# Kernel optimization log

Measured on AMD Instinct MI355X. Metric: run time of the kernel, lower is better.

The kernel has to match this reference:

```python
import jax, jax.numpy as jnp
import numpy as np

C, M, D, B, BG_KNN = 8, 2048, 2048, 256, 50
TEMP, MOMENTUM = 0.05, 0.2


def setup_inputs() -> dict:
    key = jax.random.key(0)
    k1, k2, k3, k4 = jax.random.split(key, 4)
    inputs = jax.random.normal(k1, (B, D), jnp.float32)
    inputs = inputs / jnp.linalg.norm(inputs, axis=1, keepdims=True)  # ReID feats are L2-normed
    em = jax.random.normal(k2, (C * M, D), jnp.float32)
    em = em / jnp.linalg.norm(em, axis=1, keepdims=True)  # memory rows are kept unit-norm
    targets = jax.random.randint(k3, (B,), 0, M)          # global pseudo labels in [0, M)
    cams = jax.random.randint(k4, (B,), 0, C).astype(jnp.int32)
    return {"inputs": inputs, "em": em, "targets": targets, "cams": cams, "epoch": 6}


def _loss(inputs, em_sg, targets, cams, epoch):
    em3 = em_sg.reshape(C, M, D)
    loss = jnp.zeros((), jnp.float32)
    # per-camera intra-camera cross entropy (ExemplarMemory fwd: inputs @ em.T / temp)
    for cc in range(C):
        mask = (cams == cc)
        cnt = jnp.maximum(mask.sum(), 1).astype(jnp.float32)
        logits = (inputs @ em3[cc].T) / TEMP                       # [B, M]
        logp = jax.nn.log_softmax(logits, axis=1)
        ce = -jnp.take_along_axis(logp, targets[:, None], axis=1)[:, 0]
        loss = loss + jnp.where(mask.any(), jnp.where(mask, ce, 0.0).sum() / cnt, 0.0)
    if epoch >= 5:
        sims = inputs @ em_sg.T                                    # [B, C*M]
        # positives: one proxy per camera at row target + M*c
        pos_ind = targets[:, None] + M * jnp.arange(C)[None, :]    # [B, C]
        pos_logits = jnp.take_along_axis(sims, pos_ind, axis=1) / TEMP
        masked = jax.lax.stop_gradient(sims).at[jnp.arange(B)[:, None], pos_ind].set(-1000.0)
        _, neg_ind = jax.lax.top_k(masked, BG_KNN)                 # bg_knn hard negatives
        neg_logits = jnp.take_along_axis(sims, neg_ind, axis=1) / TEMP
        cat = jnp.concatenate([pos_logits, neg_logits], axis=1)   # [B, C+BG_KNN]
        logp = jax.nn.log_softmax(cat, axis=1)
        al = -logp[:, :C].mean(axis=1)                             # weights 1/#pos on positives
        for cc in range(C):
            mask = (cams == cc)
            cnt = jnp.maximum(mask.sum(), 1).astype(jnp.float32)
            loss = loss + jnp.where(mask.any(), 0.5 * jnp.where(mask, al, 0.0).sum() / cnt, 0.0)
    return loss


def reference(inputs, em, targets, cams, epoch):
    em_sg = jax.lax.stop_gradient(em)  # memory is a buffer: no grad flows to it in torch
    loss = _loss(inputs, em_sg, targets, cams, int(epoch))
    # sequential per-sample EMA scatter update + renorm (torch does this in backward)
    rows = cams.astype(jnp.int32) * M + targets.astype(jnp.int32)
    x_sg = jax.lax.stop_gradient(inputs)

    def step(em_cur, xr):
        x, r = xr
        row = MOMENTUM * em_cur[r] + (1.0 - MOMENTUM) * x
        row = row / jnp.linalg.norm(row)
        return em_cur.at[r].set(row), None

    em_new, _ = jax.lax.scan(step, em_sg, (x_sg, rows))
    return loss, em_new
```

## Files before the change

### kernel.cpp

```cpp
#include <hip/hip_runtime.h>

#define Bn   256
#define Dk   2048
#define Cc   8
#define Mm   2048
#define Nn   16384
#define BG   50
#define INV_T 20.0f
#define NEG_INF -3.0e38f

typedef __attribute__((ext_vector_type(8))) short bf16x8;
typedef __attribute__((ext_vector_type(4))) float f32x4;

__device__ inline short f2bf(float f) {
  unsigned u = __builtin_bit_cast(unsigned, f);
  u = (u + 0x7fffu + ((u >> 16) & 1u)) >> 16;
  return (short)u;
}

__global__ __launch_bounds__(256) void prep_kernel(const int* __restrict__ cams,
                                                   float* __restrict__ loss,
                                                   int* __restrict__ cnt) {
  int t = threadIdx.x;
  if (t < Cc) cnt[t] = 0;
  if (t == 0) loss[0] = 0.0f;
  __syncthreads();
  atomicAdd(&cnt[cams[t]], 1);
}

__global__ __launch_bounds__(256) void convert_kernel(const float* __restrict__ x,
                                                      short* __restrict__ a, int n4) {
  int i = blockIdx.x * 256 + threadIdx.x;
  if (i < n4) {
    float4 v = ((const float4*)x)[i];
    short4 h;
    h.x = f2bf(v.x); h.y = f2bf(v.y); h.z = f2bf(v.z); h.w = f2bf(v.w);
    ((short4*)a)[i] = h;
  }
}

#define BK 32
#define BN 64
#define SA 40
__global__ __launch_bounds__(512) void gemm_copy_kernel(const short* __restrict__ A,
                                                        const float* __restrict__ Em,
                                                        float* __restrict__ sims,
                                                        float* __restrict__ out_em) {
  __shared__ __align__(16) short As[Bn * SA];
  __shared__ __align__(16) short Bs[BN * SA];
  const int tid = threadIdx.x;
  const int nbase = blockIdx.x * BN;
  const int lane = tid & 63;
  const int w = tid >> 6;
  const int wm = w & 3;
  const int wn = w >> 2;
  const int lr = lane & 15;
  const int lq = lane >> 4;

  f32x4 acc[4][2];
#pragma unroll
  for (int mi = 0; mi < 4; ++mi)
#pragma unroll
    for (int ni = 0; ni < 2; ++ni) acc[mi][ni] = (f32x4)(0.0f);

  const int brow = tid >> 3, bseg = tid & 7;
  for (int kt = 0; kt < Dk / BK; ++kt) {
#pragma unroll
    for (int c = 0; c < 2; ++c) {
      int l = tid + c * 512;
      int row = l >> 2, seg = l & 3;
      uint4 va = *(const uint4*)(A + (size_t)row * Dk + kt * BK + seg * 8);
      *(uint4*)(As + row * SA + seg * 8) = va;
    }
    {
      size_t go = (size_t)(nbase + brow) * Dk + kt * BK + bseg * 4;
      float4 vb = *(const float4*)(Em + go);
      short4 hb;
      hb.x = f2bf(vb.x); hb.y = f2bf(vb.y); hb.z = f2bf(vb.z); hb.w = f2bf(vb.w);
      *(short4*)(Bs + brow * SA + bseg * 4) = hb;
      out_em[go + 0] = vb.x; out_em[go + 1] = vb.y;
      out_em[go + 2] = vb.z; out_em[go + 3] = vb.w;
    }
    __syncthreads();
    bf16x8 af[4], bfr[2];
#pragma unroll
    for (int mi = 0; mi < 4; ++mi)
      af[mi] = *(const bf16x8*)(As + (wm * 64 + mi * 16 + lr) * SA + lq * 8);
#pragma unroll
    for (int ni = 0; ni < 2; ++ni)
      bfr[ni] = *(const bf16x8*)(Bs + (wn * 32 + ni * 16 + lr) * SA + lq * 8);
#pragma unroll
    for (int mi = 0; mi < 4; ++mi)
#pragma unroll
      for (int ni = 0; ni < 2; ++ni)
        acc[mi][ni] = __builtin_amdgcn_mfma_f32_16x16x32_bf16(af[mi], bfr[ni], acc[mi][ni], 0, 0, 0);
    __syncthreads();
  }
#pragma unroll
  for (int mi = 0; mi < 4; ++mi)
#pragma unroll
    for (int ni = 0; ni < 2; ++ni)
#pragma unroll
      for (int r = 0; r < 4; ++r) {
        int m = wm * 64 + mi * 16 + lq * 4 + r;
        int n = nbase + wn * 32 + ni * 16 + lr;
        sims[(size_t)m * Nn + n] = acc[mi][ni][r];
      }
}

__global__ __launch_bounds__(64) void loss_kernel(const float* __restrict__ sims,
                                                  const int* __restrict__ targets,
                                                  const int* __restrict__ cams,
                                                  const int* __restrict__ cnt,
                                                  const int* __restrict__ epoch,
                                                  float* __restrict__ loss_out) {
  __shared__ __align__(16) float row[Nn];
  const int b = blockIdx.x, tid = threadIdx.x;
  {
    const float4* src = (const float4*)(sims + (size_t)b * Nn);
    float4* dst = (float4*)row;
    for (int i = tid; i < Nn / 4; i += 64) dst[i] = src[i];
  }
  __syncthreads();
  const int cam = cams[b], tgt = targets[b];
  const int cv = cnt[cam];
  const float invc = 1.0f / (float)(cv > 0 ? cv : 1);
  const int base = cam * Mm;
  float lm = NEG_INF;
  for (int i = tid; i < Mm; i += 64) lm = fmaxf(lm, row[base + i]);
#pragma unroll
  for (int off = 32; off; off >>= 1) lm = fmaxf(lm, __shfl_down(lm, off, 64));
  const float maxv = __shfl(lm, 0, 64);
  float ls = 0.0f;
  for (int i = tid; i < Mm; i += 64) ls += __expf((row[base + i] - maxv) * INV_T);
#pragma unroll
  for (int off = 32; off; off >>= 1) ls += __shfl_down(ls, off, 64);
  const float sumexp = __shfl(ls, 0, 64);
  float total = (__logf(sumexp) + (maxv - row[base + tgt]) * INV_T) * invc;

  if (*epoch >= 5) {
    float pv[Cc];
#pragma unroll
    for (int c = 0; c < Cc; ++c) pv[c] = row[tgt + Mm * c];
    __syncthreads();
    if (tid < Cc) row[tgt + Mm * tid] = NEG_INF;
    __syncthreads();
    float mp = NEG_INF;
#pragma unroll
    for (int c = 0; c < Cc; ++c) mp = fmaxf(mp, pv[c]);
    float cand_v; int cand_i;
    {
      float v = NEG_INF; int ii = 0;
      const float4* r4 = (const float4*)row;
      for (int j = 0; j < 64; ++j) {
        int i4 = tid * 64 + j;
        float4 x = r4[i4];
        if (x.x > v) { v = x.x; ii = i4 * 4 + 0; }
        if (x.y > v) { v = x.y; ii = i4 * 4 + 1; }
        if (x.z > v) { v = x.z; ii = i4 * 4 + 2; }
        if (x.w > v) { v = x.w; ii = i4 * 4 + 3; }
      }
      cand_v = v; cand_i = ii;
    }
    float cm = 0.0f, cs = 0.0f;
    for (int it = 0; it < BG; ++it) {
      float v = cand_v; int ii = cand_i; int owner = tid;
#pragma unroll
      for (int off = 32; off; off >>= 1) {
        float ov = __shfl_down(v, off, 64);
        int oi = __shfl_down(ii, off, 64);
        int oo = __shfl_down(owner, off, 64);
        if (ov > v) { v = ov; ii = oi; owner = oo; }
      }
      v = __shfl(v, 0, 64); ii = __shfl(ii, 0, 64); owner = __shfl(owner, 0, 64);
      if (it == 0) cm = fmaxf(mp, v);
      cs += __expf((v - cm) * INV_T);
      if (tid == 0) row[ii] = NEG_INF;
      __syncthreads();
      {
        int i4 = owner * 64 + tid;
        float4 x = ((const float4*)row)[i4];
        float nv = NEG_INF; int ni = 0;
        if (x.x > nv) { nv = x.x; ni = i4 * 4 + 0; }
        if (x.y > nv) { nv = x.y; ni = i4 * 4 + 1; }
        if (x.z > nv) { nv = x.z; ni = i4 * 4 + 2; }
        if (x.w > nv) { nv = x.w; ni = i4 * 4 + 3; }
#pragma unroll
        for (int off = 32; off; off >>= 1) {
          float ov = __shfl_down(nv, off, 64);
          int oi = __shfl_down(ni, off, 64);
          if (ov > nv) { nv = ov; ni = oi; }
        }
        nv = __shfl(nv, 0, 64); ni = __shfl(ni, 0, 64);
        if (tid == owner) { cand_v = nv; cand_i = ni; }
      }
      __syncthreads();
    }
#pragma unroll
    for (int c = 0; c < Cc; ++c) cs += __expf((pv[c] - cm) * INV_T);
    const float lse = cm * INV_T + __logf(cs);
    float al = 0.0f;
#pragma unroll
    for (int c = 0; c < Cc; ++c) al += pv[c] * INV_T - lse;
    al = -al * 0.125f;
    total += 0.5f * al * invc;
  }
  if (tid == 0) atomicAdd(loss_out, total);
}

__global__ __launch_bounds__(256) void ema_kernel(const float* __restrict__ em,
                                                  const float* __restrict__ inputs,
                                                  const int* __restrict__ targets,
                                                  const int* __restrict__ cams,
                                                  float* __restrict__ out_em) {
  const int b = blockIdx.x, tid = threadIdx.x;
  const int r = cams[b] * Mm + targets[b];
  for (int j = 0; j < b; ++j)
    if (cams[j] * Mm + targets[j] == r) return;
  __shared__ float red[4];
  float v[8];
#pragma unroll
  for (int u = 0; u < 8; ++u) v[u] = em[(size_t)r * Dk + u * 256 + tid];
  const int lane = tid & 63, w = tid >> 6;
  for (int j = b; j < Bn; ++j) {
    if (cams[j] * Mm + targets[j] != r) continue;
#pragma unroll
    for (int u = 0; u < 8; ++u)
      v[u] = 0.2f * v[u] + 0.8f * inputs[(size_t)j * Dk + u * 256 + tid];
    float ss = 0.0f;
#pragma unroll
    for (int u = 0; u < 8; ++u) ss += v[u] * v[u];
#pragma unroll
    for (int off = 32; off; off >>= 1) ss += __shfl_down(ss, off, 64);
    if (lane == 0) red[w] = ss;
    __syncthreads();
    const float inv = 1.0f / sqrtf(red[0] + red[1] + red[2] + red[3]);
#pragma unroll
    for (int u = 0; u < 8; ++u) v[u] *= inv;
    __syncthreads();
  }
#pragma unroll
  for (int u = 0; u < 8; ++u) out_em[(size_t)r * Dk + u * 256 + tid] = v[u];
}

extern "C" void kernel_launch(void* const* d_in, const int* in_sizes, int n_in,
                              void* d_out, int out_size, void* d_ws, size_t ws_size,
                              hipStream_t stream) {
  const float* inputs  = (const float*)d_in[0];
  const float* em      = (const float*)d_in[1];
  const int*   targets = (const int*)d_in[2];
  const int*   cams    = (const int*)d_in[3];
  const int*   epoch   = (const int*)d_in[4];
  float* loss   = (float*)d_out;
  float* out_em = (float*)d_out + 1;

  float* sims  = (float*)d_ws;
  short* a16   = (short*)((char*)d_ws + (size_t)Bn * Nn * 4);
  int*   cnt   = (int*)((char*)d_ws + (size_t)Bn * Nn * 4 + (size_t)Bn * Dk * 2);

  hipLaunchKernelGGL(prep_kernel,    dim3(1),   dim3(256), 0, stream, cams, loss, cnt);
  hipLaunchKernelGGL(convert_kernel, dim3(512), dim3(256), 0, stream, inputs, a16, Bn * Dk / 4);
  hipLaunchKernelGGL(gemm_copy_kernel, dim3(Nn / BN), dim3(512), 0, stream, a16, em, sims, out_em);
  hipLaunchKernelGGL(loss_kernel,    dim3(Bn),  dim3(64),  0, stream, sims, targets, cams, cnt, epoch, loss);
  hipLaunchKernelGGL(ema_kernel,     dim3(Bn),  dim3(256), 0, stream, em, inputs, targets, cams, out_em);
}
```

Before: 399.3 us.

## Replace iterative top-k with radix threshold select and double-buffer GEMM tiles

The loss kernel now keeps each sims row in registers as order-preserving unsigned keys. It finds the 50th-largest negative by a 32-step bitwise radix search with block-wide counts, replacing the 50 serial argmax iterations over shared memory, and handles ties by adding copies of the threshold value. The GEMM stages A and B through double-buffered LDS with register prefetch, drops one barrier per k-step, and reads A from a pre-tiled layout written by the convert kernel. Duplicate-row detection for the EMA moves into the prep kernel, and the loss is reduced deterministically through per-row partials plus a finalize kernel instead of atomics. The register-resident row raises register pressure, and the radix search adds 32 block reductions, each with barriers.

```diff
diff --git a/kernel.cpp b/kernel.cpp
--- a/kernel.cpp
+++ b/kernel.cpp
@@ -1,13 +1,12 @@
 #include <hip/hip_runtime.h>
 
-#define Bn   256
-#define Dk   2048
-#define Cc   8
-#define Mm   2048
-#define Nn   16384
-#define BG   50
+#define Bn 256
+#define Dk 2048
+#define Cc 8
+#define Mm 2048
+#define Nn 16384
+#define BG 50
 #define INV_T 20.0f
-#define NEG_INF -3.0e38f
 
 typedef __attribute__((ext_vector_type(8))) short bf16x8;
 typedef __attribute__((ext_vector_type(4))) float f32x4;
@@ -17,45 +16,61 @@
   u = (u + 0x7fffu + ((u >> 16) & 1u)) >> 16;
   return (short)u;
 }
+__device__ inline unsigned f2ord(float f) {
+  unsigned u = __builtin_bit_cast(unsigned, f);
+  return (u & 0x80000000u) ? ~u : (u | 0x80000000u);
+}
+__device__ inline float ord2f(unsigned o) {
+  unsigned u = (o & 0x80000000u) ? (o ^ 0x80000000u) : ~o;
+  return __builtin_bit_cast(float, u);
+}
 
 __global__ __launch_bounds__(256) void prep_kernel(const int* __restrict__ cams,
-                                                   float* __restrict__ loss,
-                                                   int* __restrict__ cnt) {
-  int t = threadIdx.x;
-  if (t < Cc) cnt[t] = 0;
-  if (t == 0) loss[0] = 0.0f;
-  __syncthreads();
-  atomicAdd(&cnt[cams[t]], 1);
+                                                   const int* __restrict__ targets,
+                                                   int* __restrict__ cnt,
+                                                   int* __restrict__ rowArr,
+                                                   int* __restrict__ first) {
+  __shared__ int rs[Bn];
+  __shared__ int lc[Cc];
+  const int t = threadIdx.x;
+  const int r = cams[t] * Mm + targets[t];
+  rs[t] = r;
+  if (t < Cc) lc[t] = 0;
+  __syncthreads();
+  atomicAdd(&lc[cams[t]], 1);
+  __syncthreads();
+  if (t < Cc) cnt[t] = lc[t];
+  int fst = 1;
+  for (int j = 0; j < t; ++j)
+    if (rs[j] == r) fst = 0;
+  rowArr[t] = r;
+  first[t] = fst;
 }
 
 __global__ __launch_bounds__(256) void convert_kernel(const float* __restrict__ x,
                                                       short* __restrict__ a, int n4) {
   int i = blockIdx.x * 256 + threadIdx.x;
-  if (i < n4) {
-    float4 v = ((const float4*)x)[i];
-    short4 h;
-    h.x = f2bf(v.x); h.y = f2bf(v.y); h.z = f2bf(v.z); h.w = f2bf(v.w);
-    ((short4*)a)[i] = h;
-  }
-}
-
-#define BK 32
-#define BN 64
+  if (i >= n4) return;
+  float4 v = ((const float4*)x)[i];
+  int row = i >> 9, j = i & 511;
+  int kt = j >> 3, off = (j & 7) * 4;
+  short4 h;
+  h.x = f2bf(v.x); h.y = f2bf(v.y); h.z = f2bf(v.z); h.w = f2bf(v.w);
+  *(short4*)(a + (size_t)kt * (Bn * 32) + row * 32 + off) = h;
+}
+
 #define SA 40
 __global__ __launch_bounds__(512) void gemm_copy_kernel(const short* __restrict__ A,
                                                         const float* __restrict__ Em,
                                                         float* __restrict__ sims,
                                                         float* __restrict__ out_em) {
-  __shared__ __align__(16) short As[Bn * SA];
-  __shared__ __align__(16) short Bs[BN * SA];
+  __shared__ __align__(16) short As[2][Bn * SA];
+  __shared__ __align__(16) short Bs[2][64 * SA];
   const int tid = threadIdx.x;
-  const int nbase = blockIdx.x * BN;
+  const int nbase = blockIdx.x * 64;
   const int lane = tid & 63;
-  const int w = tid >> 6;
-  const int wm = w & 3;
-  const int wn = w >> 2;
-  const int lr = lane & 15;
-  const int lq = lane >> 4;
+  const int w = tid >> 6, wm = w & 3, wn = w >> 2;
+  const int lr = lane & 15, lq = lane >> 4;
 
   f32x4 acc[4][2];
 #pragma unroll
@@ -63,38 +78,50 @@
 #pragma unroll
     for (int ni = 0; ni < 2; ++ni) acc[mi][ni] = (f32x4)(0.0f);
 
-  const int brow = tid >> 3, bseg = tid & 7;
-  for (int kt = 0; kt < Dk / BK; ++kt) {
-#pragma unroll
-    for (int c = 0; c < 2; ++c) {
-      int l = tid + c * 512;
-      int row = l >> 2, seg = l & 3;
-      uint4 va = *(const uint4*)(A + (size_t)row * Dk + kt * BK + seg * 8);
-      *(uint4*)(As + row * SA + seg * 8) = va;
-    }
+  const int arow0 = tid >> 2, achk = (tid & 3) * 8;
+  const int brow = tid >> 3, bcol = (tid & 7) * 4;
+  const size_t bgo_base = (size_t)(nbase + brow) * Dk + bcol;
+
+  uint4 aReg0, aReg1;
+  float4 bReg;
+  aReg0 = *(const uint4*)(A + tid * 8);
+  aReg1 = *(const uint4*)(A + (tid + 512) * 8);
+  bReg = *(const float4*)(Em + bgo_base);
+
+  for (int kt = 0; kt < 64; ++kt) {
+    short* as = As[kt & 1];
+    short* bs = Bs[kt & 1];
+    *(uint4*)(as + arow0 * SA + achk) = aReg0;
+    *(uint4*)(as + (arow0 + 128) * SA + achk) = aReg1;
+    short4 hb;
+    hb.x = f2bf(bReg.x); hb.y = f2bf(bReg.y); hb.z = f2bf(bReg.z); hb.w = f2bf(bReg.w);
+    *(short4*)(bs + brow * SA + bcol) = hb;
     {
-      size_t go = (size_t)(nbase + brow) * Dk + kt * BK + bseg * 4;
-      float4 vb = *(const float4*)(Em + go);
-      short4 hb;
-      hb.x = f2bf(vb.x); hb.y = f2bf(vb.y); hb.z = f2bf(vb.z); hb.w = f2bf(vb.w);
-      *(short4*)(Bs + brow * SA + bseg * 4) = hb;
-      out_em[go + 0] = vb.x; out_em[go + 1] = vb.y;
-      out_em[go + 2] = vb.z; out_em[go + 3] = vb.w;
+      size_t go = bgo_base + (size_t)kt * 32;
+      out_em[go + 0] = bReg.x;
+      out_em[go + 1] = bReg.y;
+      out_em[go + 2] = bReg.z;
+      out_em[go + 3] = bReg.w;
     }
     __syncthreads();
+    if (kt < 63) {
+      const short* ap = A + (size_t)(kt + 1) * (Bn * 32);
+      aReg0 = *(const uint4*)(ap + tid * 8);
+      aReg1 = *(const uint4*)(ap + (tid + 512) * 8);
+      bReg = *(const float4*)(Em + bgo_base + (size_t)(kt + 1) * 32);
+    }
     bf16x8 af[4], bfr[2];
 #pragma unroll
     for (int mi = 0; mi < 4; ++mi)
-      af[mi] = *(const bf16x8*)(As + (wm * 64 + mi * 16 + lr) * SA + lq * 8);
+      af[mi] = *(const bf16x8*)(as + (wm * 64 + mi * 16 + lr) * SA + lq * 8);
 #pragma unroll
     for (int ni = 0; ni < 2; ++ni)
-      bfr[ni] = *(const bf16x8*)(Bs + (wn * 32 + ni * 16 + lr) * SA + lq * 8);
+      bfr[ni] = *(const bf16x8*)(bs + (wn * 32 + ni * 16 + lr) * SA + lq * 8);
 #pragma unroll
     for (int mi = 0; mi < 4; ++mi)
 #pragma unroll
       for (int ni = 0; ni < 2; ++ni)
         acc[mi][ni] = __builtin_amdgcn_mfma_f32_16x16x32_bf16(af[mi], bfr[ni], acc[mi][ni], 0, 0, 0);
-    __syncthreads();
   }
 #pragma unroll
   for (int mi = 0; mi < 4; ++mi)
@@ -108,122 +135,199 @@
       }
 }
 
-__global__ __launch_bounds__(64) void loss_kernel(const float* __restrict__ sims,
-                                                  const int* __restrict__ targets,
-                                                  const int* __restrict__ cams,
-                                                  const int* __restrict__ cnt,
-                                                  const int* __restrict__ epoch,
-                                                  float* __restrict__ loss_out) {
-  __shared__ __align__(16) float row[Nn];
-  const int b = blockIdx.x, tid = threadIdx.x;
+__device__ inline float blockRedSumF(float v, float* red, int tid) {
+#pragma unroll
+  for (int off = 32; off; off >>= 1) v += __shfl_down(v, off, 64);
+  if ((tid & 63) == 0) red[tid >> 6] = v;
+  __syncthreads();
+  float r = red[0] + red[1] + red[2] + red[3];
+  __syncthreads();
+  return r;
+}
+__device__ inline int blockRedSumI(int v, int* red, int tid) {
+#pragma unroll
+  for (int off = 32; off; off >>= 1) v += __shfl_down(v, off, 64);
+  if ((tid & 63) == 0) red[tid >> 6] = v;
+  __syncthreads();
+  int r = red[0] + red[1] + red[2] + red[3];
+  __syncthreads();
+  return r;
+}
+__device__ inline float blockRedMaxF(float v, float* red, int tid) {
+#pragma unroll
+  for (int off = 32; off; off >>= 1) v = fmaxf(v, __shfl_down(v, off, 64));
+  if ((tid & 63) == 0) red[tid >> 6] = v;
+  __syncthreads();
+  float r = fmaxf(fmaxf(red[0], red[1]), fmaxf(red[2], red[3]));
+  __syncthreads();
+  return r;
+}
+__device__ inline unsigned blockRedMaxU(unsigned v, unsigned* red, int tid) {
+#pragma unroll
+  for (int off = 32; off; off >>= 1) { unsigned o = __shfl_down(v, off, 64); v = o > v ? o : v; }
+  if ((tid & 63) == 0) red[tid >> 6] = v;
+  __syncthreads();
+  unsigned r = red[0];
+  r = red[1] > r ? red[1] : r; r = red[2] > r ? red[2] : r; r = red[3] > r ? red[3] : r;
+  __syncthreads();
+  return r;
+}
+
+__global__ __launch_bounds__(256) void loss_kernel(const float* __restrict__ sims,
+                                                   const int* __restrict__ targets,
+                                                   const int* __restrict__ cams,
+                                                   const int* __restrict__ cnt,
+                                                   const int* __restrict__ epoch,
+                                                   float* __restrict__ lossPartial) {
+  __shared__ float redf[4];
+  __shared__ int redi[4];
+  __shared__ unsigned redu[4];
+  __shared__ unsigned pordS[Cc];
+  const int b = blockIdx.x, t = threadIdx.x;
+
+  uint4 uarr[16];
   {
     const float4* src = (const float4*)(sims + (size_t)b * Nn);
-    float4* dst = (float4*)row;
-    for (int i = tid; i < Nn / 4; i += 64) dst[i] = src[i];
-  }
-  __syncthreads();
+#pragma unroll
+    for (int q = 0; q < 16; ++q) {
+      float4 v = src[q * 256 + t];
+      uarr[q].x = f2ord(v.x); uarr[q].y = f2ord(v.y);
+      uarr[q].z = f2ord(v.z); uarr[q].w = f2ord(v.w);
+    }
+  }
   const int cam = cams[b], tgt = targets[b];
-  const int cv = cnt[cam];
-  const float invc = 1.0f / (float)(cv > 0 ? cv : 1);
-  const int base = cam * Mm;
-  float lm = NEG_INF;
-  for (int i = tid; i < Mm; i += 64) lm = fmaxf(lm, row[base + i]);
-#pragma unroll
-  for (int off = 32; off; off >>= 1) lm = fmaxf(lm, __shfl_down(lm, off, 64));
-  const float maxv = __shfl(lm, 0, 64);
+  const int cg = cnt[cam];
+  const float invc = 1.0f / (float)(cg > 0 ? cg : 1);
+
+  {
+    const int owner = (tgt >> 2) & 255;
+    if (t == owner) {
+      const int slot = tgt & 3;
+#pragma unroll
+      for (int c = 0; c < Cc; ++c) {
+        const int chunk = (tgt >> 10) + 2 * c;
+        uint4 uc = uarr[0];
+#pragma unroll
+        for (int q = 1; q < 16; ++q)
+          if (chunk == q) uc = uarr[q];
+        unsigned po = uc.x;
+        if (slot == 1) po = uc.y;
+        else if (slot == 2) po = uc.z;
+        else if (slot == 3) po = uc.w;
+        pordS[c] = po;
+      }
+    }
+  }
+  __syncthreads();
+  unsigned pord[Cc];
+  float pv[Cc];
+#pragma unroll
+  for (int c = 0; c < Cc; ++c) { pord[c] = pordS[c]; pv[c] = ord2f(pord[c]); }
+
+  float cv[8];
+  {
+    uint4 u0 = uarr[0], u1 = uarr[1];
+#pragma unroll
+    for (int q = 0; q < 16; ++q) {
+      if (2 * cam == q) u0 = uarr[q];
+      if (2 * cam + 1 == q) u1 = uarr[q];
+    }
+    cv[0] = ord2f(u0.x); cv[1] = ord2f(u0.y); cv[2] = ord2f(u0.z); cv[3] = ord2f(u0.w);
+    cv[4] = ord2f(u1.x); cv[5] = ord2f(u1.y); cv[6] = ord2f(u1.z); cv[7] = ord2f(u1.w);
+  }
+  float lm = cv[0];
+#pragma unroll
+  for (int k = 1; k < 8; ++k) lm = fmaxf(lm, cv[k]);
+  const float maxv = blockRedMaxF(lm, redf, t);
   float ls = 0.0f;
-  for (int i = tid; i < Mm; i += 64) ls += __expf((row[base + i] - maxv) * INV_T);
-#pragma unroll
-  for (int off = 32; off; off >>= 1) ls += __shfl_down(ls, off, 64);
-  const float sumexp = __shfl(ls, 0, 64);
-  float total = (__logf(sumexp) + (maxv - row[base + tgt]) * INV_T) * invc;
+#pragma unroll
+  for (int k = 0; k < 8; ++k) ls += __expf((cv[k] - maxv) * INV_T);
+  const float sumexp = blockRedSumF(ls, redf, t);
+  float total = (__logf(sumexp) + (maxv - pv[cam]) * INV_T) * invc;
 
   if (*epoch >= 5) {
-    float pv[Cc];
-#pragma unroll
-    for (int c = 0; c < Cc; ++c) pv[c] = row[tgt + Mm * c];
-    __syncthreads();
-    if (tid < Cc) row[tgt + Mm * tid] = NEG_INF;
-    __syncthreads();
-    float mp = NEG_INF;
-#pragma unroll
-    for (int c = 0; c < Cc; ++c) mp = fmaxf(mp, pv[c]);
-    float cand_v; int cand_i;
-    {
-      float v = NEG_INF; int ii = 0;
-      const float4* r4 = (const float4*)row;
-      for (int j = 0; j < 64; ++j) {
-        int i4 = tid * 64 + j;
-        float4 x = r4[i4];
-        if (x.x > v) { v = x.x; ii = i4 * 4 + 0; }
-        if (x.y > v) { v = x.y; ii = i4 * 4 + 1; }
-        if (x.z > v) { v = x.z; ii = i4 * 4 + 2; }
-        if (x.w > v) { v = x.w; ii = i4 * 4 + 3; }
-      }
-      cand_v = v; cand_i = ii;
-    }
-    float cm = 0.0f, cs = 0.0f;
-    for (int it = 0; it < BG; ++it) {
-      float v = cand_v; int ii = cand_i; int owner = tid;
-#pragma unroll
-      for (int off = 32; off; off >>= 1) {
-        float ov = __shfl_down(v, off, 64);
-        int oi = __shfl_down(ii, off, 64);
-        int oo = __shfl_down(owner, off, 64);
-        if (ov > v) { v = ov; ii = oi; owner = oo; }
-      }
-      v = __shfl(v, 0, 64); ii = __shfl(ii, 0, 64); owner = __shfl(owner, 0, 64);
-      if (it == 0) cm = fmaxf(mp, v);
-      cs += __expf((v - cm) * INV_T);
-      if (tid == 0) row[ii] = NEG_INF;
-      __syncthreads();
-      {
-        int i4 = owner * 64 + tid;
-        float4 x = ((const float4*)row)[i4];
-        float nv = NEG_INF; int ni = 0;
-        if (x.x > nv) { nv = x.x; ni = i4 * 4 + 0; }
-        if (x.y > nv) { nv = x.y; ni = i4 * 4 + 1; }
-        if (x.z > nv) { nv = x.z; ni = i4 * 4 + 2; }
-        if (x.w > nv) { nv = x.w; ni = i4 * 4 + 3; }
-#pragma unroll
-        for (int off = 32; off; off >>= 1) {
-          float ov = __shfl_down(nv, off, 64);
-          int oi = __shfl_down(ni, off, 64);
-          if (ov > nv) { nv = ov; ni = oi; }
-        }
-        nv = __shfl(nv, 0, 64); ni = __shfl(ni, 0, 64);
-        if (tid == owner) { cand_v = nv; cand_i = ni; }
-      }
-      __syncthreads();
-    }
-#pragma unroll
-    for (int c = 0; c < Cc; ++c) cs += __expf((pv[c] - cm) * INV_T);
-    const float lse = cm * INV_T + __logf(cs);
-    float al = 0.0f;
-#pragma unroll
-    for (int c = 0; c < Cc; ++c) al += pv[c] * INV_T - lse;
-    al = -al * 0.125f;
+    unsigned cur = 0u;
+#pragma unroll 1
+    for (int bit = 31; bit >= 0; --bit) {
+      const unsigned cand = cur | (1u << bit);
+      int c = 0;
+#pragma unroll
+      for (int q = 0; q < 16; ++q)
+        c += (uarr[q].x >= cand) + (uarr[q].y >= cand) + (uarr[q].z >= cand) + (uarr[q].w >= cand);
+      int ctot = blockRedSumI(c, redi, t);
+#pragma unroll
+      for (int cc2 = 0; cc2 < Cc; ++cc2) ctot -= (pord[cc2] >= cand);
+      if (ctot >= BG) cur = cand;
+    }
+    int cg2 = 0;
+#pragma unroll
+    for (int q = 0; q < 16; ++q)
+      cg2 += (uarr[q].x > cur) + (uarr[q].y > cur) + (uarr[q].z > cur) + (uarr[q].w > cur);
+    int cgt = blockRedSumI(cg2, redi, t);
+#pragma unroll
+    for (int cc2 = 0; cc2 < Cc; ++cc2) cgt -= (pord[cc2] > cur);
+    unsigned um = 0u;
+#pragma unroll
+    for (int q = 0; q < 16; ++q) {
+      um = uarr[q].x > um ? uarr[q].x : um;
+      um = uarr[q].y > um ? uarr[q].y : um;
+      um = uarr[q].z > um ? uarr[q].z : um;
+      um = uarr[q].w > um ? uarr[q].w : um;
+    }
+    const unsigned umax = blockRedMaxU(um, redu, t);
+    const float m = ord2f(umax);
+    const float v50 = ord2f(cur);
+    float s = 0.0f;
+#pragma unroll
+    for (int q = 0; q < 16; ++q) {
+      if (uarr[q].x > cur) s += __expf((ord2f(uarr[q].x) - m) * INV_T);
+      if (uarr[q].y > cur) s += __expf((ord2f(uarr[q].y) - m) * INV_T);
+      if (uarr[q].z > cur) s += __expf((ord2f(uarr[q].z) - m) * INV_T);
+      if (uarr[q].w > cur) s += __expf((ord2f(uarr[q].w) - m) * INV_T);
+    }
+    float S = blockRedSumF(s, redf, t);
+    float psum = 0.0f;
+#pragma unroll
+    for (int cc2 = 0; cc2 < Cc; ++cc2) {
+      if (pord[cc2] > cur) S -= __expf((pv[cc2] - m) * INV_T);
+      S += __expf((pv[cc2] - m) * INV_T);
+      psum += pv[cc2];
+    }
+    S += (float)(BG - cgt) * __expf((v50 - m) * INV_T);
+    const float lse = m * INV_T + __logf(S);
+    const float al = lse - psum * (INV_T / 8.0f);
     total += 0.5f * al * invc;
   }
-  if (tid == 0) atomicAdd(loss_out, total);
+  if (t == 0) lossPartial[b] = total;
+}
+
+__global__ __launch_bounds__(256) void finalize_kernel(const float* __restrict__ lossPartial,
+                                                       float* __restrict__ loss) {
+  __shared__ float redf[4];
+  const int t = threadIdx.x;
+  float v = lossPartial[t];
+  const float r = blockRedSumF(v, redf, t);
+  if (t == 0) loss[0] = r;
 }
 
 __global__ __launch_bounds__(256) void ema_kernel(const float* __restrict__ em,
                                                   const float* __restrict__ inputs,
-                                                  const int* __restrict__ targets,
-                                                  const int* __restrict__ cams,
+                                                  const int* __restrict__ rowArr,
+                                                  const int* __restrict__ first,
                                                   float* __restrict__ out_em) {
   const int b = blockIdx.x, tid = threadIdx.x;
-  const int r = cams[b] * Mm + targets[b];
-  for (int j = 0; j < b; ++j)
-    if (cams[j] * Mm + targets[j] == r) return;
+  if (!first[b]) return;
+  const int r = rowArr[b];
+  __shared__ int rows[Bn];
   __shared__ float red[4];
+  rows[tid] = rowArr[tid];
+  __syncthreads();
   float v[8];
 #pragma unroll
   for (int u = 0; u < 8; ++u) v[u] = em[(size_t)r * Dk + u * 256 + tid];
   const int lane = tid & 63, w = tid >> 6;
   for (int j = b; j < Bn; ++j) {
-    if (cams[j] * Mm + targets[j] != r) continue;
+    if (rows[j] != r) continue;
 #pragma unroll
     for (int u = 0; u < 8; ++u)
       v[u] = 0.2f * v[u] + 0.8f * inputs[(size_t)j * Dk + u * 256 + tid];
@@ -254,13 +358,18 @@
   float* loss   = (float*)d_out;
   float* out_em = (float*)d_out + 1;
 
-  float* sims  = (float*)d_ws;
-  short* a16   = (short*)((char*)d_ws + (size_t)Bn * Nn * 4);
-  int*   cnt   = (int*)((char*)d_ws + (size_t)Bn * Nn * 4 + (size_t)Bn * Dk * 2);
-
-  hipLaunchKernelGGL(prep_kernel,    dim3(1),   dim3(256), 0, stream, cams, loss, cnt);
-  hipLaunchKernelGGL(convert_kernel, dim3(512), dim3(256), 0, stream, inputs, a16, Bn * Dk / 4);
-  hipLaunchKernelGGL(gemm_copy_kernel, dim3(Nn / BN), dim3(512), 0, stream, a16, em, sims, out_em);
-  hipLaunchKernelGGL(loss_kernel,    dim3(Bn),  dim3(64),  0, stream, sims, targets, cams, cnt, epoch, loss);
-  hipLaunchKernelGGL(ema_kernel,     dim3(Bn),  dim3(256), 0, stream, em, inputs, targets, cams, out_em);
-}
+  float* sims = (float*)d_ws;
+  short* a16  = (short*)((char*)d_ws + (size_t)Bn * Nn * 4);
+  float* lossPartial = (float*)((char*)d_ws + (size_t)Bn * Nn * 4 + (size_t)Bn * Dk * 2);
+  int* ibase  = (int*)(lossPartial + Bn);
+  int* cnt    = ibase;
+  int* rowArr = ibase + 8;
+  int* first  = ibase + 8 + Bn;
+
+  hipLaunchKernelGGL(prep_kernel,    dim3(1),       dim3(256), 0, stream, cams, targets, cnt, rowArr, first);
+  hipLaunchKernelGGL(convert_kernel, dim3(512),     dim3(256), 0, stream, inputs, a16, Bn * Dk / 4);
+  hipLaunchKernelGGL(gemm_copy_kernel, dim3(Nn / 64), dim3(512), 0, stream, a16, em, sims, out_em);
+  hipLaunchKernelGGL(loss_kernel,    dim3(Bn),      dim3(256), 0, stream, sims, targets, cams, cnt, epoch, lossPartial);
+  hipLaunchKernelGGL(finalize_kernel, dim3(1),      dim3(256), 0, stream, lossPartial, loss);
+  hipLaunchKernelGGL(ema_kernel,     dim3(Bn),      dim3(256), 0, stream, em, inputs, rowArr, first, out_em);
+}
```

New measurement: 374.6 us. 1.07x faster.
